# Optimization experiments

Measured on AMD Instinct MI355X. Metric: run time of the kernel, lower is better.

The kernel has to match this reference:

```python
import jax, jax.numpy as jnp
import numpy as np

D_MODEL = 768
N_HEAD = 12


def setup_inputs() -> dict:
    key = jax.random.key(0)
    ks = jax.random.split(key, 5)
    B, S, D = 2, 4096, D_MODEL
    scale = 0.02
    return {
        "x": jax.random.normal(ks[0], (B, S, D), dtype=jnp.float32),
        "W_in": jax.random.normal(ks[1], (D, 3 * D), dtype=jnp.float32) * scale,
        "b_in": jax.random.normal(ks[2], (3 * D,), dtype=jnp.float32) * scale,
        "W_out": jax.random.normal(ks[3], (D, D), dtype=jnp.float32) * scale,
        "b_out": jax.random.normal(ks[4], (D,), dtype=jnp.float32) * scale,
    }


def reference(x, W_in, b_in, W_out, b_out):
    B, S, D = x.shape
    H = N_HEAD
    d_head = D // H
    qkv = x @ W_in + b_in                      # [B,S,3D]
    q, k, v = jnp.split(qkv, 3, axis=-1)
    # [B,H,S,d]
    q = q.reshape(B, S, H, d_head).transpose(0, 2, 1, 3)
    k = k.reshape(B, S, H, d_head).transpose(0, 2, 1, 3)
    v = v.reshape(B, S, H, d_head).transpose(0, 2, 1, 3)
    att = jnp.einsum("bhqd,bhkd->bhqk", q, k) * (1.0 / jnp.sqrt(jnp.float32(d_head)))
    causal = jnp.tril(jnp.ones((S, S), dtype=bool))
    att = jnp.where(causal[None, None], att, jnp.float32(-jnp.inf))
    att = jax.nn.softmax(att, axis=-1)
    y = jnp.einsum("bhqk,bhkd->bhqd", att, v)  # [B,H,S,d]
    y = y.transpose(0, 2, 1, 3).reshape(B, S, D)
    return y @ W_out + b_out
```

## Files before the change

kernel.cpp:

```cpp
#include <hip/hip_runtime.h>
#include <hip/hip_bf16.h>


#define D_MODEL 768
#define SEQ 4096
#define NB 2
#define NHEAD 12

typedef __attribute__((ext_vector_type(8))) short short8;
typedef __attribute__((ext_vector_type(4))) float floatx4;
typedef __attribute__((ext_vector_type(16))) float floatx16;

#define SM_C 0.18033688011112042f

#if __has_builtin(__builtin_amdgcn_exp2f)
#define EXP2(x) __builtin_amdgcn_exp2f(x)
#else
#define EXP2(x) __expf((x) * 0.6931471805599453f)
#endif

__device__ inline short fb(float f) {
    union { __hip_bfloat16 h; short s; } cv;
    cv.h = __float2bfloat16(f);
    return cv.s;
}
__device__ inline unsigned pk2(float a, float b) {
    float2 f; f.x = a; f.y = b;
    union { __hip_bfloat162 h; unsigned u; } cv;
    cv.h = __float22bfloat162_rn(f);
    return cv.u;
}
__device__ inline void gload16(const void* g, void* l) {
    __builtin_amdgcn_global_load_lds(
        (const __attribute__((address_space(1))) unsigned int*)g,
        (__attribute__((address_space(3))) unsigned int*)l, 16, 0, 0);
}

__global__ __launch_bounds__(256) void convert_bf16(const float* __restrict__ src,
                                                    short* __restrict__ dst, size_t n) {
    size_t i = ((size_t)blockIdx.x * 256 + threadIdx.x) * 8;
    if (i >= n) return;
    float4 f0 = *(const float4*)(src + i);
    float4 f1 = *(const float4*)(src + i + 4);
    uint4 u = {pk2(f0.x, f0.y), pk2(f0.z, f0.w), pk2(f1.x, f1.y), pk2(f1.z, f1.w)};
    *(uint4*)(dst + i) = u;
}

__global__ __launch_bounds__(256) void transpose_bf16(const float* __restrict__ W,
                                                      short* __restrict__ Wt,
                                                      int K, int N) {
    __shared__ short t[32][33];
    const int n0 = blockIdx.x * 32, k0 = blockIdx.y * 32;
    const int tx = threadIdx.x, ty = threadIdx.y;
#pragma unroll
    for (int j = 0; j < 4; ++j)
        t[ty + j * 8][tx] = fb(W[(size_t)(k0 + ty + j * 8) * N + n0 + tx]);
    __syncthreads();
#pragma unroll
    for (int j = 0; j < 4; ++j)
        Wt[(size_t)(n0 + ty + j * 8) * K + k0 + tx] = t[tx][ty + j * 8];
}

__global__ __launch_bounds__(256) void gemm_qkv128(const short* __restrict__ A,
                                                   const short* __restrict__ Bt,
                                                   const float* __restrict__ bias,
                                                   short* __restrict__ qw,
                                                   short* __restrict__ kblk,
                                                   short* __restrict__ vblk) {
    const int K = D_MODEL;
    __shared__ short As[128][32];
    __shared__ short Bs[128][32];
    const int tid = threadIdx.x, lane = tid & 63, w = tid >> 6;
    const int wr = w >> 1, wc = w & 1;
    const int lo = lane & 15, hi = lane >> 4;
    const int m0 = blockIdx.y * 128, n0 = blockIdx.x * 128;
    const int lr = lane >> 2, lc = (lane & 3) * 8;

    floatx4 acc[4][4] = {};
    const short* Ag = A  + (size_t)(m0 + w * 16 + lr) * K + lc;
    const short* Bg = Bt + (size_t)(n0 + w * 16 + lr) * K + lc;

    for (int k0 = 0; k0 < K; k0 += 32) {
        __syncthreads();
        gload16(Ag + k0,                  &As[w * 16][0]);
        gload16(Ag + k0 + (size_t)64 * K, &As[64 + w * 16][0]);
        gload16(Bg + k0,                  &Bs[w * 16][0]);
        gload16(Bg + k0 + (size_t)64 * K, &Bs[64 + w * 16][0]);
        __syncthreads();
        short8 a[4], bf[4];
#pragma unroll
        for (int m = 0; m < 4; ++m) a[m] = *(const short8*)&As[wr * 64 + m * 16 + lo][hi * 8];
#pragma unroll
        for (int n = 0; n < 4; ++n) bf[n] = *(const short8*)&Bs[wc * 64 + n * 16 + lo][hi * 8];
#pragma unroll
        for (int m = 0; m < 4; ++m)
#pragma unroll
            for (int n = 0; n < 4; ++n)
                acc[m][n] = __builtin_amdgcn_mfma_f32_16x16x32_bf16(a[m], bf[n], acc[m][n], 0, 0, 0);
    }

#pragma unroll
    for (int m = 0; m < 4; ++m)
#pragma unroll
        for (int n = 0; n < 4; ++n) {
            int col  = n0 + wc * 64 + n * 16 + lo;
            int row0 = m0 + wr * 64 + m * 16 + hi * 4;
            float bv = bias[col];
            if (col < D_MODEL) {
#pragma unroll
                for (int r = 0; r < 4; ++r)
                    qw[(size_t)(row0 + r) * D_MODEL + col] = fb((acc[m][n][r] + bv) * SM_C);
            } else if (col < 2 * D_MODEL) {
                int kc2 = col - D_MODEL;
                int hh = kc2 >> 6, dh = kc2 & 63;
#pragma unroll
                for (int r = 0; r < 4; ++r) {
                    int row = row0 + r;
                    int bb = row >> 12, s = row & 4095;
                    int kb = s >> 6, kr = s & 63;
                    size_t base = (((size_t)bb * NHEAD + hh) * 64 + kb) * 4096;
                    kblk[base + kr * 64 + (((dh >> 3) ^ (kr & 7)) * 8) + (dh & 7)] =
                        fb(acc[m][n][r] + bv);
                }
            } else {
                int vcol = col - 2 * D_MODEL;
                int hh = vcol >> 6, dh = vcol & 63;
                int bb = row0 >> 12, s = row0 & 4095;
                int kb = s >> 6, kr = s & 63;
                size_t base = (((size_t)bb * NHEAD + hh) * 64 + kb) * 4096;
                uint2 u = {pk2(acc[m][n][0] + bv, acc[m][n][1] + bv),
                           pk2(acc[m][n][2] + bv, acc[m][n][3] + bv)};
                *(uint2*)&vblk[base + dh * 64 + (((kr >> 3) ^ (dh & 7)) * 8) + (kr & 7)] = u;
            }
        }
}

__global__ __launch_bounds__(256) void gemm_out128(const short* __restrict__ A,
                                                   const short* __restrict__ Bt,
                                                   const float* __restrict__ bias,
                                                   float* __restrict__ C) {
    const int K = D_MODEL, N = D_MODEL;
    __shared__ short As[128][32];
    __shared__ short Bs[128][32];
    const int tid = threadIdx.x, lane = tid & 63, w = tid >> 6;
    const int wr = w >> 1, wc = w & 1;
    const int lo = lane & 15, hi = lane >> 4;
    const int m0 = blockIdx.y * 128, n0 = blockIdx.x * 128;
    const int lr = lane >> 2, lc = (lane & 3) * 8;

    floatx4 acc[4][4] = {};
    const short* Ag = A  + (size_t)(m0 + w * 16 + lr) * K + lc;
    const short* Bg = Bt + (size_t)(n0 + w * 16 + lr) * K + lc;

    for (int k0 = 0; k0 < K; k0 += 32) {
        __syncthreads();
        gload16(Ag + k0,                  &As[w * 16][0]);
        gload16(Ag + k0 + (size_t)64 * K, &As[64 + w * 16][0]);
        gload16(Bg + k0,                  &Bs[w * 16][0]);
        gload16(Bg + k0 + (size_t)64 * K, &Bs[64 + w * 16][0]);
        __syncthreads();
        short8 a[4], bf[4];
#pragma unroll
        for (int m = 0; m < 4; ++m) a[m] = *(const short8*)&As[wr * 64 + m * 16 + lo][hi * 8];
#pragma unroll
        for (int n = 0; n < 4; ++n) bf[n] = *(const short8*)&Bs[wc * 64 + n * 16 + lo][hi * 8];
#pragma unroll
        for (int m = 0; m < 4; ++m)
#pragma unroll
            for (int n = 0; n < 4; ++n)
                acc[m][n] = __builtin_amdgcn_mfma_f32_16x16x32_bf16(a[m], bf[n], acc[m][n], 0, 0, 0);
    }

#pragma unroll
    for (int m = 0; m < 4; ++m)
#pragma unroll
        for (int n = 0; n < 4; ++n) {
            int col  = n0 + wc * 64 + n * 16 + lo;
            int row0 = m0 + wr * 64 + m * 16 + hi * 4;
            float bv = bias[col];
#pragma unroll
            for (int r = 0; r < 4; ++r)
                C[(size_t)(row0 + r) * N + col] = acc[m][n][r] + bv;
        }
}

__global__ __launch_bounds__(256, 3) void attn_k(const short* __restrict__ qw,
                                                 const short* __restrict__ kblk,
                                                 const short* __restrict__ vblk,
                                                 short* __restrict__ y) {
    const int L = blockIdx.x;
    const int xcd = L & 7, slot = L >> 3;
    const int ghead = slot >> 5, ip = slot & 31;
    const int g = ghead * 8 + xcd;
    const int b = g / NHEAD, h = g % NHEAD;

    const int tid = threadIdx.x, lane = tid & 63, w = tid >> 6;
    const int q32 = lane & 31, hh = lane >> 5;
    const int pairB = w >> 1;
    const int wp = w & 1;
    const int wrow = wp * 32;

    __shared__ alignas(16) short KVs[2][2][64 * 64];
    __shared__ float Lcmb[128];

    const short* qbase = qw + (size_t)b * SEQ * D_MODEL;
    const short* kimg = kblk + (((size_t)b * NHEAD + h) * 64) * 4096;
    const short* vimg = vblk + (((size_t)b * NHEAD + h) * 64) * 4096;

    short* Kb = KVs[pairB][0];
    short* Vb = KVs[pairB][1];

    const short* kSrc = kimg + wp * 2048 + lane * 8;
    const short* vSrc = vimg + wp * 2048 + lane * 8;
    short* kDst = Kb + wp * 2048;
    short* vDst = Vb + wp * 2048;

    const int qt_hi = 63 - ip, qt_lo = ip;
    int tq0 = (pairB ? qt_lo : qt_hi) * 64;

    short8 qf[4];
    {
        const short* qr = qbase + (size_t)(tq0 + wrow + q32) * D_MODEL + h * 64 + hh * 8;
        qf[0] = *(const short8*)(qr);
        qf[1] = *(const short8*)(qr + 16);
        qf[2] = *(const short8*)(qr + 32);
        qf[3] = *(const short8*)(qr + 48);
    }

    floatx16 O0 = {}, O1 = {};
    float lsum = 0.0f;

    auto store_out = [&](float ltot) {
        float inv = 1.0f / ltot;
#pragma unroll
        for (int r = 0; r < 16; ++r) {
            int qrow = (r & 3) + 8 * (r >> 2) + 4 * hh;
            float iv = __shfl(inv, qrow, 64);
            short* d = y + ((size_t)b * SEQ + tq0 + wrow + qrow) * D_MODEL + h * 64;
            d[q32]      = fb(O0[r] * iv);
            d[32 + q32] = fb(O1[r] * iv);
        }
    };

    for (int j = 0; j <= 32; ++j) {
        int myblk;
        if (!pairB) myblk = j;
        else        myblk = (j <= ip) ? j : (j <= 31 ? 32 + (j - ip) : -1);

        __syncthreads();
        if (myblk >= 0) {
            const short* ks = kSrc + (size_t)myblk * 4096;
            const short* vs = vSrc + (size_t)myblk * 4096;
#pragma unroll
            for (int c = 0; c < 4; ++c) {
                gload16(ks + c * 512, kDst + c * 512);
                gload16(vs + c * 512, vDst + c * 512);
            }
        }
        __syncthreads();

        if (pairB && j == ip + 1) {
            float ltot = lsum + __shfl_xor(lsum, 32, 64);
            store_out(ltot);
#pragma unroll
            for (int r = 0; r < 16; ++r) { O0[r] = 0.0f; O1[r] = 0.0f; }
            lsum = 0.0f;
            tq0 = qt_hi * 64;
            const short* qr = qbase + (size_t)(tq0 + wrow + q32) * D_MODEL + h * 64 + hh * 8;
            qf[0] = *(const short8*)(qr);
            qf[1] = *(const short8*)(qr + 16);
            qf[2] = *(const short8*)(qr + 32);
            qf[3] = *(const short8*)(qr + 48);
        }

        if (myblk >= 0) {
            const int myqt = (pairB && j <= ip) ? qt_lo : qt_hi;
            const bool diag = (myblk == myqt);

#pragma unroll
            for (int kb2 = 0; kb2 < 2; ++kb2) {
                floatx16 S = {};
                __builtin_amdgcn_s_setprio(1);
#pragma unroll
                for (int kc = 0; kc < 4; ++kc) {
                    short8 kf = *(const short8*)&Kb[(kb2 * 32 + q32) * 64 + ((kc * 2 + hh) ^ (q32 & 7)) * 8];
                    S = __builtin_amdgcn_mfma_f32_32x32x16_bf16(kf, qf[kc], S, 0, 0, 0);
                }
                __builtin_amdgcn_s_setprio(0);

                if (diag) {
                    int qg = tq0 + wrow + q32;
                    int kb_base = myblk * 64 + kb2 * 32 + 4 * hh;
#pragma unroll
                    for (int r = 0; r < 16; ++r) {
                        int kgl = kb_base + (r & 3) + 8 * (r >> 2);
                        if (kgl > qg) S[r] = -1e30f;
                    }
                }

                unsigned wA[4], wB[4];
#pragma unroll
                for (int g4 = 0; g4 < 4; ++g4) {
                    float p0 = EXP2(S[4 * g4 + 0]), p1 = EXP2(S[4 * g4 + 1]);
                    float p2 = EXP2(S[4 * g4 + 2]), p3 = EXP2(S[4 * g4 + 3]);
                    lsum += (p0 + p1) + (p2 + p3);
                    wA[g4] = pk2(p0, p1);
                    wB[g4] = pk2(p2, p3);
                }
#pragma unroll
                for (int c16 = 0; c16 < 2; ++c16) {
                    unsigned xa = wA[2 * c16], ya = wA[2 * c16 + 1];
                    unsigned xb = wB[2 * c16], yb = wB[2 * c16 + 1];
                    asm("v_permlane32_swap_b32 %0, %1" : "+v"(xa), "+v"(ya));
                    asm("v_permlane32_swap_b32 %0, %1" : "+v"(xb), "+v"(yb));
                    union { unsigned u[4]; short8 s; } pa;
                    pa.u[0] = xa; pa.u[1] = xb; pa.u[2] = ya; pa.u[3] = yb;
                    const int kc = kb2 * 2 + c16;
                    short8 vf0 = *(const short8*)&Vb[q32 * 64 + ((kc * 2 + hh) ^ (q32 & 7)) * 8];
                    short8 vf1 = *(const short8*)&Vb[(32 + q32) * 64 + ((kc * 2 + hh) ^ (q32 & 7)) * 8];
                    __builtin_amdgcn_s_setprio(1);
                    O0 = __builtin_amdgcn_mfma_f32_32x32x16_bf16(pa.s, vf0, O0, 0, 0, 0);
                    O1 = __builtin_amdgcn_mfma_f32_32x32x16_bf16(pa.s, vf1, O1, 0, 0, 0);
                    __builtin_amdgcn_s_setprio(0);
                }
            }
        }
    }

    if (pairB) {
        float* cO = (float*)&KVs[1][0][0];
        const int lane2 = wp * 64 + lane;
#pragma unroll
        for (int r = 0; r < 16; ++r) {
            cO[r * 128 + lane2]        = O0[r];
            cO[(16 + r) * 128 + lane2] = O1[r];
        }
        Lcmb[lane2] = lsum;
    }
    __syncthreads();
    if (!pairB) {
        const float* cO = (const float*)&KVs[1][0][0];
        const int lane2 = wp * 64 + lane;
#pragma unroll
        for (int r = 0; r < 16; ++r) {
            O0[r] += cO[r * 128 + lane2];
            O1[r] += cO[(16 + r) * 128 + lane2];
        }
        lsum += Lcmb[lane2];
        float ltot = lsum + __shfl_xor(lsum, 32, 64);
        store_out(ltot);
    }
}

extern "C" void kernel_launch(void* const* d_in, const int* in_sizes, int n_in,
                              void* d_out, int out_size, void* d_ws, size_t ws_size,
                              hipStream_t stream) {
    (void)in_sizes; (void)n_in; (void)out_size; (void)ws_size;
    const float* x     = (const float*)d_in[0];
    const float* W_in  = (const float*)d_in[1];
    const float* b_in  = (const float*)d_in[2];
    const float* W_out = (const float*)d_in[3];
    const float* b_out = (const float*)d_in[4];
    float* out = (float*)d_out;

    const int M = NB * SEQ;
    char* p = (char*)d_ws;
    short* xbf   = (short*)p; p += (size_t)M * D_MODEL * 2;
    short* wtin  = (short*)p; p += (size_t)3 * D_MODEL * D_MODEL * 2;
    short* wtout = (short*)p; p += (size_t)D_MODEL * D_MODEL * 2;
    short* qw    = (short*)p; p += (size_t)M * D_MODEL * 2;
    short* kblk  = (short*)p; p += (size_t)NB * NHEAD * 64 * 4096 * 2;
    short* vblk  = (short*)p; p += (size_t)NB * NHEAD * 64 * 4096 * 2;
    short* yw    = (short*)p;

    convert_bf16<<<dim3((unsigned)((size_t)M * D_MODEL / 8 / 256)), 256, 0, stream>>>(
        x, xbf, (size_t)M * D_MODEL);
    transpose_bf16<<<dim3(3 * D_MODEL / 32, D_MODEL / 32), dim3(32, 8), 0, stream>>>(
        W_in, wtin, D_MODEL, 3 * D_MODEL);
    transpose_bf16<<<dim3(D_MODEL / 32, D_MODEL / 32), dim3(32, 8), 0, stream>>>(
        W_out, wtout, D_MODEL, D_MODEL);
    gemm_qkv128<<<dim3(3 * D_MODEL / 128, M / 128), 256, 0, stream>>>(
        xbf, wtin, b_in, qw, kblk, vblk);
    attn_k<<<dim3(NB * NHEAD * (SEQ / 128)), 256, 0, stream>>>(qw, kblk, vblk, yw);
    gemm_out128<<<dim3(D_MODEL / 128, M / 128), 256, 0, stream>>>(yw, wtout, b_out, out);
}
```

Baseline: 171.2 us.

## Double-buffer K tiles and split V wait to overlap loads with QK compute

The attention kernel now prefetches the next K block into a second LDS buffer while the current block is processed. It also issues the V load for the current block before the QK^T MFMAs and waits on V only after the softmax exponentials. The old full __syncthreads pairs are replaced with explicit vmcnt waits and raw barriers, so global-load latency is hidden behind compute. In exchange, LDS use grows by one K tile per pair (which may reduce occupancy under launch_bounds 3) and correctness now depends on hand-tuned vmcnt counts.

```diff
diff --git a/kernel.cpp b/kernel.cpp
--- a/kernel.cpp
+++ b/kernel.cpp
@@ -200,20 +200,19 @@
     const int wp = w & 1;
     const int wrow = wp * 32;
 
-    __shared__ alignas(16) short KVs[2][2][64 * 64];
+    __shared__ alignas(16) short Kdb[2][2][64 * 64];
+    __shared__ alignas(16) short Vsb[2][64 * 64];
     __shared__ float Lcmb[128];
 
     const short* qbase = qw + (size_t)b * SEQ * D_MODEL;
     const short* kimg = kblk + (((size_t)b * NHEAD + h) * 64) * 4096;
     const short* vimg = vblk + (((size_t)b * NHEAD + h) * 64) * 4096;
 
-    short* Kb = KVs[pairB][0];
-    short* Vb = KVs[pairB][1];
-
     const short* kSrc = kimg + wp * 2048 + lane * 8;
     const short* vSrc = vimg + wp * 2048 + lane * 8;
-    short* kDst = Kb + wp * 2048;
-    short* vDst = Vb + wp * 2048;
+    short* kDst0 = &Kdb[pairB][0][wp * 2048];
+    short* kDst1 = &Kdb[pairB][1][wp * 2048];
+    short* vDst  = &Vsb[pairB][wp * 2048];
 
     const int qt_hi = 63 - ip, qt_lo = ip;
     int tq0 = (pairB ? qt_lo : qt_hi) * 64;
@@ -242,22 +241,41 @@
         }
     };
 
+    auto blk_at = [&](int jj) -> int {
+        if (jj > 32) return -1;
+        if (!pairB) return jj;
+        return (jj <= ip) ? jj : (jj <= 31 ? 32 + (jj - ip) : -1);
+    };
+
+    {
+#pragma unroll
+        for (int c = 0; c < 4; ++c)
+            gload16(kSrc + c * 512, kDst0 + c * 512);
+    }
+
     for (int j = 0; j <= 32; ++j) {
-        int myblk;
-        if (!pairB) myblk = j;
-        else        myblk = (j <= ip) ? j : (j <= 31 ? 32 + (j - ip) : -1);
-
-        __syncthreads();
+        const int myblk = blk_at(j);
+        const int nblk  = blk_at(j + 1);
+
+        __builtin_amdgcn_s_barrier();
+
+        if (nblk >= 0) {
+            const short* ks = kSrc + (size_t)nblk * 4096;
+            short* kd = ((j + 1) & 1) ? kDst1 : kDst0;
+#pragma unroll
+            for (int c = 0; c < 4; ++c)
+                gload16(ks + c * 512, kd + c * 512);
+        }
         if (myblk >= 0) {
-            const short* ks = kSrc + (size_t)myblk * 4096;
             const short* vs = vSrc + (size_t)myblk * 4096;
 #pragma unroll
-            for (int c = 0; c < 4; ++c) {
-                gload16(ks + c * 512, kDst + c * 512);
+            for (int c = 0; c < 4; ++c)
                 gload16(vs + c * 512, vDst + c * 512);
-            }
-        }
-        __syncthreads();
+        }
+        if (nblk >= 0) { asm volatile("s_waitcnt vmcnt(8)" ::: "memory"); }
+        else           { asm volatile("s_waitcnt vmcnt(4)" ::: "memory"); }
+        __builtin_amdgcn_sched_barrier(0);
+        __builtin_amdgcn_s_barrier();
 
         if (pairB && j == ip + 1) {
             float ltot = lsum + __shfl_xor(lsum, 32, 64);
@@ -273,7 +291,9 @@
             qf[3] = *(const short8*)(qr + 48);
         }
 
+        unsigned wA[4], wB[4], wA2[4], wB2[4];
         if (myblk >= 0) {
+            const short* Kb = &Kdb[pairB][j & 1][0];
             const int myqt = (pairB && j <= ip) ? qt_lo : qt_hi;
             const bool diag = (myblk == myqt);
 
@@ -298,19 +318,33 @@
                     }
                 }
 
-                unsigned wA[4], wB[4];
+                unsigned* WA = kb2 ? wA2 : wA;
+                unsigned* WB = kb2 ? wB2 : wB;
 #pragma unroll
                 for (int g4 = 0; g4 < 4; ++g4) {
                     float p0 = EXP2(S[4 * g4 + 0]), p1 = EXP2(S[4 * g4 + 1]);
                     float p2 = EXP2(S[4 * g4 + 2]), p3 = EXP2(S[4 * g4 + 3]);
                     lsum += (p0 + p1) + (p2 + p3);
-                    wA[g4] = pk2(p0, p1);
-                    wB[g4] = pk2(p2, p3);
+                    WA[g4] = pk2(p0, p1);
+                    WB[g4] = pk2(p2, p3);
                 }
+            }
+        }
+        if (nblk >= 0) { asm volatile("s_waitcnt vmcnt(4)" ::: "memory"); }
+        else           { asm volatile("s_waitcnt vmcnt(0)" ::: "memory"); }
+        __builtin_amdgcn_sched_barrier(0);
+        __builtin_amdgcn_s_barrier();
+
+        if (myblk >= 0) {
+            const short* Vb = &Vsb[pairB][0];
+#pragma unroll
+            for (int kb2 = 0; kb2 < 2; ++kb2) {
+                unsigned* WA = kb2 ? wA2 : wA;
+                unsigned* WB = kb2 ? wB2 : wB;
 #pragma unroll
                 for (int c16 = 0; c16 < 2; ++c16) {
-                    unsigned xa = wA[2 * c16], ya = wA[2 * c16 + 1];
-                    unsigned xb = wB[2 * c16], yb = wB[2 * c16 + 1];
+                    unsigned xa = WA[2 * c16], ya = WA[2 * c16 + 1];
+                    unsigned xb = WB[2 * c16], yb = WB[2 * c16 + 1];
                     asm("v_permlane32_swap_b32 %0, %1" : "+v"(xa), "+v"(ya));
                     asm("v_permlane32_swap_b32 %0, %1" : "+v"(xb), "+v"(yb));
                     union { unsigned u[4]; short8 s; } pa;
@@ -328,7 +362,7 @@
     }
 
     if (pairB) {
-        float* cO = (float*)&KVs[1][0][0];
+        float* cO = (float*)&Kdb[1][0][0];
         const int lane2 = wp * 64 + lane;
 #pragma unroll
         for (int r = 0; r < 16; ++r) {
@@ -339,7 +373,7 @@
     }
     __syncthreads();
     if (!pairB) {
-        const float* cO = (const float*)&KVs[1][0][0];
+        const float* cO = (const float*)&Kdb[1][0][0];
         const int lane2 = wp * 64 + lane;
 #pragma unroll
         for (int r = 0; r < 16; ++r) {
```

New measurement: 176.3 us. 1.03x slower.

## Load K/V fragments directly from global in MFMA-ready layout, drop LDS staging

Applied to the files above, without the earlier changes.

The QKV GEMM epilogue now writes Q, K and V in a fragment-major layout where each lane's short8 is contiguous, so the attention kernel loads MFMA operands straight from global memory into registers. The LDS staging, syncthreads and cross-wave pair combination are removed. Each 128-thread block has two waves, and each wave owns one 64-row query tile, processed as two 32-row halves over its causal key blocks. The next K block is register double-buffered and the next V block is prefetched after the PV step. This trades LDS traffic and barriers for more register pressure and redundant global/L2 reads of K/V per wave. Load balance now relies on pairing tiles t and t+1 within a block, with no cross-wave work splitting.

```diff
diff --git a/kernel.cpp b/kernel.cpp
--- a/kernel.cpp
+++ b/kernel.cpp
@@ -64,9 +64,9 @@
 __global__ __launch_bounds__(256) void gemm_qkv128(const short* __restrict__ A,
                                                    const short* __restrict__ Bt,
                                                    const float* __restrict__ bias,
-                                                   short* __restrict__ qw,
-                                                   short* __restrict__ kblk,
-                                                   short* __restrict__ vblk) {
+                                                   short* __restrict__ qimg,
+                                                   short* __restrict__ kimg,
+                                                   short* __restrict__ vimg) {
     const int K = D_MODEL;
     __shared__ short As[128][32];
     __shared__ short Bs[128][32];
@@ -107,19 +107,28 @@
             int row0 = m0 + wr * 64 + m * 16 + hi * 4;
             float bv = bias[col];
             if (col < D_MODEL) {
-#pragma unroll
-                for (int r = 0; r < 4; ++r)
-                    qw[(size_t)(row0 + r) * D_MODEL + col] = fb((acc[m][n][r] + bv) * SM_C);
+                int hq = col >> 6, dh = col & 63;
+                int kc = dh >> 4, dl = (dh >> 3) & 1, d7 = dh & 7;
+#pragma unroll
+                for (int r = 0; r < 4; ++r) {
+                    int row = row0 + r;
+                    int bb = row >> 12, s = row & 4095;
+                    size_t off = (((((size_t)bb * NHEAD + hq) * 64 + (s >> 6)) * 8
+                                  + ((s >> 5) & 1) * 4 + kc) * 512)
+                               + ((s & 31) + dl * 32) * 8 + d7;
+                    qimg[off] = fb((acc[m][n][r] + bv) * SM_C);
+                }
             } else if (col < 2 * D_MODEL) {
                 int kc2 = col - D_MODEL;
                 int hh = kc2 >> 6, dh = kc2 & 63;
+                int kc = dh >> 4, dl = (dh >> 3) & 1, d7 = dh & 7;
 #pragma unroll
                 for (int r = 0; r < 4; ++r) {
                     int row = row0 + r;
                     int bb = row >> 12, s = row & 4095;
                     int kb = s >> 6, kr = s & 63;
                     size_t base = (((size_t)bb * NHEAD + hh) * 64 + kb) * 4096;
-                    kblk[base + kr * 64 + (((dh >> 3) ^ (kr & 7)) * 8) + (dh & 7)] =
+                    kimg[base + ((kr >> 5) * 4 + kc) * 512 + ((kr & 31) + dl * 32) * 8 + d7] =
                         fb(acc[m][n][r] + bv);
                 }
             } else {
@@ -128,9 +137,11 @@
                 int bb = row0 >> 12, s = row0 & 4095;
                 int kb = s >> 6, kr = s & 63;
                 size_t base = (((size_t)bb * NHEAD + hh) * 64 + kb) * 4096;
+                size_t off = base + ((dh >> 5) * 4 + (kr >> 4)) * 512
+                           + ((dh & 31) + ((kr >> 3) & 1) * 32) * 8 + (kr & 7);
                 uint2 u = {pk2(acc[m][n][0] + bv, acc[m][n][1] + bv),
                            pk2(acc[m][n][2] + bv, acc[m][n][3] + bv)};
-                *(uint2*)&vblk[base + dh * 64 + (((kr >> 3) ^ (dh & 7)) * 8) + (kr & 7)] = u;
+                *(uint2*)&vimg[off] = u;
             }
         }
 }
@@ -184,126 +195,83 @@
         }
 }
 
-__global__ __launch_bounds__(256, 3) void attn_k(const short* __restrict__ qw,
-                                                 const short* __restrict__ kblk,
-                                                 const short* __restrict__ vblk,
+__global__ __launch_bounds__(128, 2) void attn_k(const short* __restrict__ qimg,
+                                                 const short* __restrict__ kimg,
+                                                 const short* __restrict__ vimg,
                                                  short* __restrict__ y) {
     const int L = blockIdx.x;
-    const int xcd = L & 7, slot = L >> 3;
-    const int ghead = slot >> 5, ip = slot & 31;
+    const int xcd = L & 7, s = L >> 3;
+    const int ghead = s >> 5, jj = s & 31;
     const int g = ghead * 8 + xcd;
     const int b = g / NHEAD, h = g % NHEAD;
-
-    const int tid = threadIdx.x, lane = tid & 63, w = tid >> 6;
-    const int q32 = lane & 31, hh = lane >> 5;
-    const int pairB = w >> 1;
-    const int wp = w & 1;
-    const int wrow = wp * 32;
-
-    __shared__ alignas(16) short KVs[2][2][64 * 64];
-    __shared__ float Lcmb[128];
-
-    const short* qbase = qw + (size_t)b * SEQ * D_MODEL;
-    const short* kimg = kblk + (((size_t)b * NHEAD + h) * 64) * 4096;
-    const short* vimg = vblk + (((size_t)b * NHEAD + h) * 64) * 4096;
-
-    short* Kb = KVs[pairB][0];
-    short* Vb = KVs[pairB][1];
-
-    const short* kSrc = kimg + wp * 2048 + lane * 8;
-    const short* vSrc = vimg + wp * 2048 + lane * 8;
-    short* kDst = Kb + wp * 2048;
-    short* vDst = Vb + wp * 2048;
-
-    const int qt_hi = 63 - ip, qt_lo = ip;
-    int tq0 = (pairB ? qt_lo : qt_hi) * 64;
-
-    short8 qf[4];
-    {
-        const short* qr = qbase + (size_t)(tq0 + wrow + q32) * D_MODEL + h * 64 + hh * 8;
-        qf[0] = *(const short8*)(qr);
-        qf[1] = *(const short8*)(qr + 16);
-        qf[2] = *(const short8*)(qr + 32);
-        qf[3] = *(const short8*)(qr + 48);
-    }
-
-    floatx16 O0 = {}, O1 = {};
-    float lsum = 0.0f;
-
-    auto store_out = [&](float ltot) {
-        float inv = 1.0f / ltot;
-#pragma unroll
-        for (int r = 0; r < 16; ++r) {
-            int qrow = (r & 3) + 8 * (r >> 2) + 4 * hh;
-            float iv = __shfl(inv, qrow, 64);
-            short* d = y + ((size_t)b * SEQ + tq0 + wrow + qrow) * D_MODEL + h * 64;
-            d[q32]      = fb(O0[r] * iv);
-            d[32 + q32] = fb(O1[r] * iv);
-        }
-    };
-
-    for (int j = 0; j <= 32; ++j) {
-        int myblk;
-        if (!pairB) myblk = j;
-        else        myblk = (j <= ip) ? j : (j <= 31 ? 32 + (j - ip) : -1);
-
-        __syncthreads();
-        if (myblk >= 0) {
-            const short* ks = kSrc + (size_t)myblk * 4096;
-            const short* vs = vSrc + (size_t)myblk * 4096;
-#pragma unroll
-            for (int c = 0; c < 4; ++c) {
-                gload16(ks + c * 512, kDst + c * 512);
-                gload16(vs + c * 512, vDst + c * 512);
+    const int w = threadIdx.x >> 6, lane = threadIdx.x & 63;
+    const int l31 = lane & 31, hh = lane >> 5;
+
+    const int t = 2 * (31 - jj) + w;
+    const int nblk = t + 1;
+
+    const short* kbase = kimg + (((size_t)b * NHEAD + h) * 64) * 4096 + lane * 8;
+    const short* vbase = vimg + (((size_t)b * NHEAD + h) * 64) * 4096 + lane * 8;
+    const short* qbase = qimg + ((((size_t)b * NHEAD + h) * 64 + t) * 8) * 512 + lane * 8;
+
+    short8 qf0[4], qf1[4];
+#pragma unroll
+    for (int kc = 0; kc < 4; ++kc) {
+        qf0[kc] = *(const short8*)(qbase + kc * 512);
+        qf1[kc] = *(const short8*)(qbase + (4 + kc) * 512);
+    }
+
+    short8 kfA[8], kfB[8], vf[8];
+#pragma unroll
+    for (int i = 0; i < 8; ++i) {
+        kfA[i] = *(const short8*)(kbase + i * 512);
+        vf[i]  = *(const short8*)(vbase + i * 512);
+    }
+
+    floatx16 O[2][2] = {};
+    float lsum0 = 0.0f, lsum1 = 0.0f;
+
+    auto body = [&](short8 (&kcur)[8], short8 (&knxt)[8], int j) {
+        const bool more = (j + 1 < nblk);
+        if (more) {
+            const short* kp = kbase + (size_t)(j + 1) * 4096;
+#pragma unroll
+            for (int i = 0; i < 8; ++i) knxt[i] = *(const short8*)(kp + i * 512);
+        }
+        const bool diag = (j == nblk - 1);
+        const int qg0 = t * 64 + l31, qg1 = qg0 + 32;
+
+#pragma unroll
+        for (int kb2 = 0; kb2 < 2; ++kb2) {
+            floatx16 S0 = {}, S1 = {};
+            __builtin_amdgcn_s_setprio(1);
+#pragma unroll
+            for (int kc = 0; kc < 4; ++kc) {
+                S0 = __builtin_amdgcn_mfma_f32_32x32x16_bf16(kcur[kb2 * 4 + kc], qf0[kc], S0, 0, 0, 0);
+                S1 = __builtin_amdgcn_mfma_f32_32x32x16_bf16(kcur[kb2 * 4 + kc], qf1[kc], S1, 0, 0, 0);
             }
-        }
-        __syncthreads();
-
-        if (pairB && j == ip + 1) {
-            float ltot = lsum + __shfl_xor(lsum, 32, 64);
-            store_out(ltot);
-#pragma unroll
-            for (int r = 0; r < 16; ++r) { O0[r] = 0.0f; O1[r] = 0.0f; }
-            lsum = 0.0f;
-            tq0 = qt_hi * 64;
-            const short* qr = qbase + (size_t)(tq0 + wrow + q32) * D_MODEL + h * 64 + hh * 8;
-            qf[0] = *(const short8*)(qr);
-            qf[1] = *(const short8*)(qr + 16);
-            qf[2] = *(const short8*)(qr + 32);
-            qf[3] = *(const short8*)(qr + 48);
-        }
-
-        if (myblk >= 0) {
-            const int myqt = (pairB && j <= ip) ? qt_lo : qt_hi;
-            const bool diag = (myblk == myqt);
-
-#pragma unroll
-            for (int kb2 = 0; kb2 < 2; ++kb2) {
-                floatx16 S = {};
-                __builtin_amdgcn_s_setprio(1);
-#pragma unroll
-                for (int kc = 0; kc < 4; ++kc) {
-                    short8 kf = *(const short8*)&Kb[(kb2 * 32 + q32) * 64 + ((kc * 2 + hh) ^ (q32 & 7)) * 8];
-                    S = __builtin_amdgcn_mfma_f32_32x32x16_bf16(kf, qf[kc], S, 0, 0, 0);
-                }
-                __builtin_amdgcn_s_setprio(0);
-
-                if (diag) {
-                    int qg = tq0 + wrow + q32;
-                    int kb_base = myblk * 64 + kb2 * 32 + 4 * hh;
-#pragma unroll
-                    for (int r = 0; r < 16; ++r) {
-                        int kgl = kb_base + (r & 3) + 8 * (r >> 2);
-                        if (kgl > qg) S[r] = -1e30f;
-                    }
-                }
-
+            __builtin_amdgcn_s_setprio(0);
+
+            if (diag) {
+                int kb_base = j * 64 + kb2 * 32 + 4 * hh;
+#pragma unroll
+                for (int r = 0; r < 16; ++r) {
+                    int kgl = kb_base + (r & 3) + 8 * (r >> 2);
+                    if (kgl > qg0) S0[r] = -1e30f;
+                    if (kgl > qg1) S1[r] = -1e30f;
+                }
+            }
+
+#pragma unroll
+            for (int qh = 0; qh < 2; ++qh) {
+                floatx16& S = qh ? S1 : S0;
                 unsigned wA[4], wB[4];
 #pragma unroll
                 for (int g4 = 0; g4 < 4; ++g4) {
                     float p0 = EXP2(S[4 * g4 + 0]), p1 = EXP2(S[4 * g4 + 1]);
                     float p2 = EXP2(S[4 * g4 + 2]), p3 = EXP2(S[4 * g4 + 3]);
-                    lsum += (p0 + p1) + (p2 + p3);
+                    float ps = (p0 + p1) + (p2 + p3);
+                    if (qh) lsum1 += ps; else lsum0 += ps;
                     wA[g4] = pk2(p0, p1);
                     wB[g4] = pk2(p2, p3);
                 }
@@ -315,40 +283,43 @@
                     asm("v_permlane32_swap_b32 %0, %1" : "+v"(xb), "+v"(yb));
                     union { unsigned u[4]; short8 s; } pa;
                     pa.u[0] = xa; pa.u[1] = xb; pa.u[2] = ya; pa.u[3] = yb;
-                    const int kc = kb2 * 2 + c16;
-                    short8 vf0 = *(const short8*)&Vb[q32 * 64 + ((kc * 2 + hh) ^ (q32 & 7)) * 8];
-                    short8 vf1 = *(const short8*)&Vb[(32 + q32) * 64 + ((kc * 2 + hh) ^ (q32 & 7)) * 8];
+                    const int kcg = kb2 * 2 + c16;
                     __builtin_amdgcn_s_setprio(1);
-                    O0 = __builtin_amdgcn_mfma_f32_32x32x16_bf16(pa.s, vf0, O0, 0, 0, 0);
-                    O1 = __builtin_amdgcn_mfma_f32_32x32x16_bf16(pa.s, vf1, O1, 0, 0, 0);
+                    O[qh][0] = __builtin_amdgcn_mfma_f32_32x32x16_bf16(pa.s, vf[kcg],     O[qh][0], 0, 0, 0);
+                    O[qh][1] = __builtin_amdgcn_mfma_f32_32x32x16_bf16(pa.s, vf[4 + kcg], O[qh][1], 0, 0, 0);
                     __builtin_amdgcn_s_setprio(0);
                 }
             }
         }
-    }
-
-    if (pairB) {
-        float* cO = (float*)&KVs[1][0][0];
-        const int lane2 = wp * 64 + lane;
+
+        if (more) {
+            const short* vp = vbase + (size_t)(j + 1) * 4096;
+#pragma unroll
+            for (int i = 0; i < 8; ++i) vf[i] = *(const short8*)(vp + i * 512);
+        }
+    };
+
+    int j = 0;
+    while (j + 2 <= nblk) {
+        body(kfA, kfB, j);
+        body(kfB, kfA, j + 1);
+        j += 2;
+    }
+    if (j < nblk) body(kfA, kfB, j);
+
+    lsum0 += __shfl_xor(lsum0, 32, 64);
+    lsum1 += __shfl_xor(lsum1, 32, 64);
+#pragma unroll
+    for (int qh = 0; qh < 2; ++qh) {
+        float inv = 1.0f / (qh ? lsum1 : lsum0);
 #pragma unroll
         for (int r = 0; r < 16; ++r) {
-            cO[r * 128 + lane2]        = O0[r];
-            cO[(16 + r) * 128 + lane2] = O1[r];
-        }
-        Lcmb[lane2] = lsum;
-    }
-    __syncthreads();
-    if (!pairB) {
-        const float* cO = (const float*)&KVs[1][0][0];
-        const int lane2 = wp * 64 + lane;
-#pragma unroll
-        for (int r = 0; r < 16; ++r) {
-            O0[r] += cO[r * 128 + lane2];
-            O1[r] += cO[(16 + r) * 128 + lane2];
-        }
-        lsum += Lcmb[lane2];
-        float ltot = lsum + __shfl_xor(lsum, 32, 64);
-        store_out(ltot);
+            int qrow = (r & 3) + 8 * (r >> 2) + 4 * hh;
+            float iv = __shfl(inv, qrow, 64);
+            short* d = y + ((size_t)b * SEQ + t * 64 + qh * 32 + qrow) * D_MODEL + h * 64;
+            d[l31]      = fb(O[qh][0][r] * iv);
+            d[32 + l31] = fb(O[qh][1][r] * iv);
+        }
     }
 }
 
@@ -368,9 +339,9 @@
     short* xbf   = (short*)p; p += (size_t)M * D_MODEL * 2;
     short* wtin  = (short*)p; p += (size_t)3 * D_MODEL * D_MODEL * 2;
     short* wtout = (short*)p; p += (size_t)D_MODEL * D_MODEL * 2;
-    short* qw    = (short*)p; p += (size_t)M * D_MODEL * 2;
-    short* kblk  = (short*)p; p += (size_t)NB * NHEAD * 64 * 4096 * 2;
-    short* vblk  = (short*)p; p += (size_t)NB * NHEAD * 64 * 4096 * 2;
+    short* qimg  = (short*)p; p += (size_t)M * D_MODEL * 2;
+    short* kimg  = (short*)p; p += (size_t)NB * NHEAD * 64 * 4096 * 2;
+    short* vimg  = (short*)p; p += (size_t)NB * NHEAD * 64 * 4096 * 2;
     short* yw    = (short*)p;
 
     convert_bf16<<<dim3((unsigned)((size_t)M * D_MODEL / 8 / 256)), 256, 0, stream>>>(
@@ -380,7 +351,7 @@
     transpose_bf16<<<dim3(D_MODEL / 32, D_MODEL / 32), dim3(32, 8), 0, stream>>>(
         W_out, wtout, D_MODEL, D_MODEL);
     gemm_qkv128<<<dim3(3 * D_MODEL / 128, M / 128), 256, 0, stream>>>(
-        xbf, wtin, b_in, qw, kblk, vblk);
-    attn_k<<<dim3(NB * NHEAD * (SEQ / 128)), 256, 0, stream>>>(qw, kblk, vblk, yw);
+        xbf, wtin, b_in, qimg, kimg, vimg);
+    attn_k<<<dim3(NB * NHEAD * 32), 128, 0, stream>>>(qimg, kimg, vimg, yw);
     gemm_out128<<<dim3(D_MODEL / 128, M / 128), 256, 0, stream>>>(yw, wtout, b_out, out);
 }
```

Result: slower. 428.4 us (+150.3%).
